# Kernel tuning notes

Measured on AMD Instinct MI355X. Metric: run time of the kernel, lower is better.

The kernel has to match this reference:

```python
import jax, jax.numpy as jnp
import numpy as np

N_MIN = 5
N_MAX = 16
VARIANTS_PER_N = 16
NUM_HIDDEN = 2
HIDDEN = 512
TOTAL_MODELS = (N_MAX - N_MIN + 1) * VARIANTS_PER_N  # 192
BATCH = 65536


def setup_inputs() -> dict:
    key = jax.random.key(0)
    ks = jax.random.split(key, 8)
    n = 16
    s_in = 1.0 / np.sqrt(n)
    s_h = 1.0 / np.sqrt(HIDDEN)
    return {
        "T": jax.random.normal(ks[0], (BATCH, n), dtype=jnp.float32),
        "n": n,
        "variant_index": 3,
        "w_in": jax.random.normal(ks[1], (TOTAL_MODELS, HIDDEN, N_MAX), dtype=jnp.float32) * s_in,
        "b_in": jax.random.normal(ks[2], (TOTAL_MODELS, HIDDEN), dtype=jnp.float32) * 0.01,
        "w_hid": jax.random.normal(ks[3], (TOTAL_MODELS, NUM_HIDDEN, HIDDEN, HIDDEN), dtype=jnp.float32) * s_h,
        "b_hid": jax.random.normal(ks[4], (TOTAL_MODELS, NUM_HIDDEN, HIDDEN), dtype=jnp.float32) * 0.01,
        "w_out": jax.random.normal(ks[5], (TOTAL_MODELS, N_MAX + 1, HIDDEN), dtype=jnp.float32) * s_h,
        "b_out": jax.random.normal(ks[6], (TOTAL_MODELS, N_MAX + 1), dtype=jnp.float32) * 0.01,
    }


def _distortion(X, n):
    # X: (B, n+1). Z[:, n-1-i] = sum_j X[:, j] * X[:, j+i+1] (zero-padded shift).
    # lag k = i+1 -> column n-k; loop is over fixed small n (<=16), unrolls statically.
    cols = [jnp.sum(X[:, :-k] * X[:, k:], axis=1) for k in range(1, n + 1)]
    return jnp.stack(cols[::-1], axis=1)  # (B, n)


def reference(T, n, variant_index, w_in, b_in, w_hid, b_hid, w_out, b_out):
    model_idx = (n - N_MIN) * VARIANTS_PER_N + variant_index
    wi = w_in[model_idx]    # (H, N_MAX)
    bi = b_in[model_idx]    # (H,)
    wh = w_hid[model_idx]   # (2, H, H)
    bh = b_hid[model_idx]   # (2, H)
    wo = w_out[model_idx]   # (N_MAX+1, H)
    bo = b_out[model_idx]   # (N_MAX+1,)

    T_pad = jnp.pad(T, ((0, 0), (0, N_MAX - n)))  # (B, N_MAX)
    norm = jnp.sqrt(jnp.clip(jnp.sum(T_pad * T_pad, axis=1, keepdims=True), 1e-12))
    T_unit = T_pad / norm
    scale = jnp.sqrt(norm)

    x = jax.nn.silu(T_unit @ wi.T + bi)
    for h in range(NUM_HIDDEN):
        x = jax.nn.relu(x @ wh[h].T + bh[h])
    x_full = (x @ wo.T + bo) * scale  # (B, N_MAX+1)

    X_hat = x_full[:, :n + 1]
    X_hat_clamped = jnp.clip(X_hat, -2.0, 2.0)
    error = jnp.mean((_distortion(X_hat, n) - T) ** 2)
    error_clamped = jnp.mean((_distortion(X_hat_clamped, n) - T) ** 2)
    return (X_hat, error, X_hat_clamped, error_clamped)
```

## Files before the change

kernel.cpp:

```cpp
#include <hip/hip_runtime.h>

#define BATCH 65536
#define MT 64

typedef unsigned short u16;
typedef __bf16 bf16x8 __attribute__((ext_vector_type(8)));
typedef float f32x4 __attribute__((ext_vector_type(4)));

#define WI_OFF 0
#define WH_OFF 16384
#define WO_OFF 540672
#define WS_USH 557056
#define BI_F 0
#define BH_F 512
#define BO_F 1536
#define ERR_F 1568
#define PREP_WH 65536
#define PREP_WI 2048
#define PREP_WO 2048
#define PREP_SC 1570
#define PREP_TOTAL (PREP_WH + PREP_WI + PREP_WO + PREP_SC)

__device__ inline u16 f2bf(float f) {
  union { float f; unsigned u; } v; v.f = f;
  unsigned u = v.u + 0x7fffu + ((v.u >> 16) & 1u);
  return (u16)(u >> 16);
}

__global__ void prep_kernel(const float* __restrict__ w_in, const float* __restrict__ b_in,
                            const float* __restrict__ w_hid, const float* __restrict__ b_hid,
                            const float* __restrict__ w_out, const float* __restrict__ b_out,
                            const int* __restrict__ variant, int n,
                            u16* __restrict__ wsu, float* __restrict__ wsf)
{
  const int model = (n - 5) * 16 + variant[0];
  const int i = blockIdx.x * 256 + threadIdx.x;
  if (i < PREP_WH) {
    int g = i & 3, col = (i >> 2) & 511, K32 = (i >> 11) & 15, l = i >> 15;
    const float* src = w_hid + (size_t)model * 524288 + (size_t)l * 262144 + col * 512 + K32 * 32 + g * 8;
    u16* dst = wsu + WH_OFF + (size_t)i * 8;
    #pragma unroll
    for (int e = 0; e < 8; ++e) dst[e] = f2bf(src[e]);
  } else if (i < PREP_WH + PREP_WI) {
    int j = i - PREP_WH;
    int g = j & 3, col = j >> 2;
    u16* dst = wsu + WI_OFF + (size_t)j * 8;
    #pragma unroll
    for (int e = 0; e < 8; ++e) {
      int k = g * 8 + e;
      dst[e] = (k < 16) ? f2bf(w_in[(size_t)model * 8192 + col * 16 + k]) : (u16)0;
    }
  } else if (i < PREP_WH + PREP_WI + PREP_WO) {
    int j = i - PREP_WH - PREP_WI;
    int g = j & 3, col = (j >> 2) & 31, K32 = j >> 7;
    u16* dst = wsu + WO_OFF + (size_t)j * 8;
    #pragma unroll
    for (int e = 0; e < 8; ++e) {
      int k = K32 * 32 + g * 8 + e;
      dst[e] = (col < 17) ? f2bf(w_out[(size_t)model * 8704 + col * 512 + k]) : (u16)0;
    }
  } else if (i < PREP_TOTAL) {
    int j = i - PREP_WH - PREP_WI - PREP_WO;
    if (j < 512)       wsf[BI_F + j] = b_in[(size_t)model * 512 + j];
    else if (j < 1536) wsf[BH_F + (j - 512)] = b_hid[(size_t)model * 1024 + (j - 512)];
    else if (j < 1568) { int o = j - 1536; wsf[BO_F + o] = (o < 17) ? b_out[(size_t)model * 17 + o] : 0.f; }
    else               wsf[ERR_F + (j - 1568)] = 0.f;
  }
}

__device__ __forceinline__ bf16x8 rdA(const char* xb, int row, int kbyte) {
  return *reinterpret_cast<const bf16x8*>(xb + row * 1024 + (kbyte ^ ((row & 15) << 4)));
}
__device__ __forceinline__ void st16(char* xb, int row, int col, u16 v) {
  *(u16*)(xb + row * 1024 + ((col * 2) ^ ((row & 15) << 4))) = v;
}

template<int NK>
__device__ __forceinline__ void dense_layer(const u16* __restrict__ Wp,
                                            const float* __restrict__ bias, int act,
                                            char* xb, int l15, int q, int c0)
{
  f32x4 acc[4][4];
  #pragma unroll
  for (int a = 0; a < 4; ++a)
    #pragma unroll
    for (int b = 0; b < 4; ++b) { f32x4 z = {0.f, 0.f, 0.f, 0.f}; acc[a][b] = z; }

  const u16* Wl = Wp + (c0 + l15) * 32 + q * 8;
  uint4 b0[4], b1[4];
  #pragma unroll
  for (int ct = 0; ct < 4; ++ct)
    b0[ct] = *reinterpret_cast<const uint4*>(Wl + ct * 512);

  #pragma unroll
  for (int K2 = 0; K2 < NK; K2 += 2) {
    if (K2 + 1 < NK) {
      #pragma unroll
      for (int ct = 0; ct < 4; ++ct)
        b1[ct] = *reinterpret_cast<const uint4*>(Wl + (K2 + 1) * 16384 + ct * 512);
    }
    {
      const int kbyte = K2 * 64 + q * 16;
      #pragma unroll
      for (int mt = 0; mt < 4; ++mt) {
        bf16x8 a = rdA(xb, mt * 16 + l15, kbyte);
        #pragma unroll
        for (int ct = 0; ct < 4; ++ct)
          acc[mt][ct] = __builtin_amdgcn_mfma_f32_16x16x32_bf16(
              a, __builtin_bit_cast(bf16x8, b0[ct]), acc[mt][ct], 0, 0, 0);
      }
    }
    if (K2 + 1 < NK) {
      if (K2 + 2 < NK) {
        #pragma unroll
        for (int ct = 0; ct < 4; ++ct)
          b0[ct] = *reinterpret_cast<const uint4*>(Wl + (K2 + 2) * 16384 + ct * 512);
      }
      const int kbyte = (K2 + 1) * 64 + q * 16;
      #pragma unroll
      for (int mt = 0; mt < 4; ++mt) {
        bf16x8 a = rdA(xb, mt * 16 + l15, kbyte);
        #pragma unroll
        for (int ct = 0; ct < 4; ++ct)
          acc[mt][ct] = __builtin_amdgcn_mfma_f32_16x16x32_bf16(
              a, __builtin_bit_cast(bf16x8, b1[ct]), acc[mt][ct], 0, 0, 0);
      }
    }
  }
  __syncthreads();

  float bv[4];
  #pragma unroll
  for (int ct = 0; ct < 4; ++ct) bv[ct] = bias[c0 + ct * 16 + l15];
  #pragma unroll
  for (int mt = 0; mt < 4; ++mt)
    #pragma unroll
    for (int ct = 0; ct < 4; ++ct)
      #pragma unroll
      for (int j = 0; j < 4; ++j) {
        int row = mt * 16 + q * 4 + j;
        float z = acc[mt][ct][j] + bv[ct];
        float h = act ? fmaxf(z, 0.f) : z / (1.f + __expf(-z));
        st16(xb, row, c0 + ct * 16 + l15, f2bf(h));
      }
  __syncthreads();
}

template<int CN>
__global__ __launch_bounds__(512, 2) void fused_kernel(
    const float* __restrict__ T, const u16* __restrict__ wsu,
    const float* __restrict__ wsf, float* __restrict__ Xout, float* __restrict__ Xcout,
    float* __restrict__ errAcc, int n_arg)
{
  const int n = CN ? CN : n_arg;
  __shared__ u16 xs[MT * 512];
  __shared__ float xo[MT * 20];
  __shared__ float scaleS[MT];
  __shared__ float ered[8][2];

  const int tid = threadIdx.x;
  const int blk = blockIdx.x;
  const int lane = tid & 63;
  const int wid = tid >> 6;
  const int l15 = lane & 15;
  const int q = lane >> 4;
  const int c0 = wid * 64;
  char* xb = (char*)xs;

  {
    const int r = tid >> 3, j = tid & 7;
    const size_t gr = (size_t)blk * MT + r;
    const float* tp = T + gr * n;
    const int k0 = 2 * j, k1 = 2 * j + 1;
    float v0 = (k0 < n) ? tp[k0] : 0.f;
    float v1 = (k1 < n) ? tp[k1] : 0.f;
    float ss = v0 * v0 + v1 * v1;
    ss += __shfl_xor(ss, 1); ss += __shfl_xor(ss, 2); ss += __shfl_xor(ss, 4);
    float norm = sqrtf(ss < 1e-12f ? 1e-12f : ss);
    float rn = 1.f / norm;
    if (j == 0) scaleS[r] = sqrtf(norm);
    st16(xb, r, k0, f2bf(v0 * rn));
    st16(xb, r, k1, f2bf(v1 * rn));
    st16(xb, r, 16 + k0, 0);
    st16(xb, r, 16 + k1, 0);
  }
  __syncthreads();

  dense_layer<1 >(wsu + WI_OFF,          wsf + BI_F,       0, xb, l15, q, c0);
  dense_layer<16>(wsu + WH_OFF,          wsf + BH_F,       1, xb, l15, q, c0);
  dense_layer<16>(wsu + WH_OFF + 262144, wsf + BH_F + 512, 1, xb, l15, q, c0);

  if (wid < 4) {
    f32x4 oacc[2];
    { f32x4 z = {0.f, 0.f, 0.f, 0.f}; oacc[0] = z; oacc[1] = z; }
    const int bofs2 = l15 * 32 + q * 8;
    uint4 ob[2], on[2];
    #pragma unroll
    for (int ct = 0; ct < 2; ++ct)
      ob[ct] = *reinterpret_cast<const uint4*>(wsu + WO_OFF + bofs2 + ct * 512);
    #pragma unroll
    for (int K2 = 0; K2 < 16; K2 += 2) {
      #pragma unroll
      for (int ct = 0; ct < 2; ++ct)
        on[ct] = *reinterpret_cast<const uint4*>(wsu + WO_OFF + (K2 + 1) * 1024 + bofs2 + ct * 512);
      {
        bf16x8 a = rdA(xb, wid * 16 + l15, K2 * 64 + q * 16);
        #pragma unroll
        for (int ct = 0; ct < 2; ++ct)
          oacc[ct] = __builtin_amdgcn_mfma_f32_16x16x32_bf16(
              a, __builtin_bit_cast(bf16x8, ob[ct]), oacc[ct], 0, 0, 0);
      }
      if (K2 + 2 < 16) {
        #pragma unroll
        for (int ct = 0; ct < 2; ++ct)
          ob[ct] = *reinterpret_cast<const uint4*>(wsu + WO_OFF + (K2 + 2) * 1024 + bofs2 + ct * 512);
      }
      {
        bf16x8 a = rdA(xb, wid * 16 + l15, (K2 + 1) * 64 + q * 16);
        #pragma unroll
        for (int ct = 0; ct < 2; ++ct)
          oacc[ct] = __builtin_amdgcn_mfma_f32_16x16x32_bf16(
              a, __builtin_bit_cast(bf16x8, on[ct]), oacc[ct], 0, 0, 0);
      }
    }
    #pragma unroll
    for (int ct = 0; ct < 2; ++ct)
      #pragma unroll
      for (int j = 0; j < 4; ++j) {
        int o = ct * 16 + l15;
        int row = wid * 16 + q * 4 + j;
        if (o <= n) {
          float val = (oacc[ct][j] + wsf[BO_F + o]) * scaleS[row];
          size_t gr = (size_t)blk * MT + row;
          float cv = fminf(fmaxf(val, -2.f), 2.f);
          Xout[gr * (n + 1) + o] = val;
          Xcout[gr * (n + 1) + o] = cv;
          xo[row * 20 + o] = val;
        }
      }
  }
  __syncthreads();

  {
    const int r = tid >> 3, j = tid & 7;
    const size_t gr = (size_t)blk * MT + r;
    float x[17], cx[17];
    #pragma unroll
    for (int i = 0; i < 17; ++i) {
      float v = (i <= n) ? xo[r * 20 + i] : 0.f;
      x[i] = v; cx[i] = fminf(fmaxf(v, -2.f), 2.f);
    }
    float e = 0.f, ec = 0.f;
    #pragma unroll
    for (int kk = 0; kk < 2; ++kk) {
      int k = j + 1 + kk * 8;
      if (k <= n) {
        float d = 0.f, dc = 0.f;
        #pragma unroll
        for (int i = 0; i < 16; ++i) {
          if (i + k <= 16) {
            if (i + k <= n) { d += x[i] * x[i + k]; dc += cx[i] * cx[i + k]; }
          }
        }
        float tvv = T[gr * n + (n - k)];
        float r1 = d - tvv, r2 = dc - tvv;
        e += r1 * r1; ec += r2 * r2;
      }
    }
    e += __shfl_xor(e, 1);  ec += __shfl_xor(ec, 1);
    e += __shfl_xor(e, 2);  ec += __shfl_xor(ec, 2);
    e += __shfl_xor(e, 4);  ec += __shfl_xor(ec, 4);
    e += __shfl_xor(e, 8);  ec += __shfl_xor(ec, 8);
    e += __shfl_xor(e, 16); ec += __shfl_xor(ec, 16);
    e += __shfl_xor(e, 32); ec += __shfl_xor(ec, 32);
    if (lane == 0) { ered[wid][0] = e; ered[wid][1] = ec; }
  }
  __syncthreads();
  if (tid == 0) {
    float e = 0.f, ec = 0.f;
    #pragma unroll
    for (int w = 0; w < 8; ++w) { e += ered[w][0]; ec += ered[w][1]; }
    atomicAdd(&errAcc[0], e);
    atomicAdd(&errAcc[1], ec);
  }
}

__global__ void finalize_kernel(const float* __restrict__ errAcc, float* __restrict__ e0,
                                float* __restrict__ e1, float inv)
{
  e0[0] = errAcc[0] * inv;
  e1[0] = errAcc[1] * inv;
}

extern "C" void kernel_launch(void* const* d_in, const int* in_sizes, int n_in,
                              void* d_out, int out_size, void* d_ws, size_t ws_size,
                              hipStream_t stream)
{
  const float* T       = (const float*)d_in[0];
  const int*   variant = (const int*)d_in[2];
  const float* w_in    = (const float*)d_in[3];
  const float* b_in    = (const float*)d_in[4];
  const float* w_hid   = (const float*)d_in[5];
  const float* b_hid   = (const float*)d_in[6];
  const float* w_out   = (const float*)d_in[7];
  const float* b_out   = (const float*)d_in[8];
  const int n = in_sizes[0] / BATCH;

  u16* wsu = (u16*)d_ws;
  float* wsf = (float*)((char*)d_ws + (size_t)WS_USH * 2);
  float* out = (float*)d_out;
  const size_t xe = (size_t)BATCH * (n + 1);
  float* Xo  = out;
  float* eP  = out + xe;
  float* Xc  = out + xe + 1;
  float* ecP = out + 2 * xe + 1;

  const int prepBlocks = (PREP_TOTAL + 255) / 256;
  prep_kernel<<<prepBlocks, 256, 0, stream>>>(w_in, b_in, w_hid, b_hid, w_out, b_out,
                                              variant, n, wsu, wsf);
  if (n == 16)
    fused_kernel<16><<<BATCH / MT, 512, 0, stream>>>(T, wsu, wsf, Xo, Xc, wsf + ERR_F, n);
  else
    fused_kernel<0><<<BATCH / MT, 512, 0, stream>>>(T, wsu, wsf, Xo, Xc, wsf + ERR_F, n);
  finalize_kernel<<<1, 1, 0, stream>>>(wsf + ERR_F, eP, ecP, 1.f / (float)((size_t)BATCH * n));
}
```

Baseline: 139.0 us.

## Double row tile to 128 with 1024-thread blocks and stagger K order per block

The row tile grows from 64 to 128. Blocks now run 1024 threads as 16 waves arranged as two row halves by eight column slices, so each weight fragment loaded into registers is shared across twice as many rows per block. The K iteration order in the hidden layers is rotated by a per-block offset, spreading concurrent blocks over different parts of the weight matrix in cache. The costs are double the LDS per block, which limits occupancy to about one block per CU. The aggressive launch bounds may also force register limits or spills.

```diff
diff --git a/kernel.cpp b/kernel.cpp
--- a/kernel.cpp
+++ b/kernel.cpp
@@ -1,7 +1,7 @@
 #include <hip/hip_runtime.h>
 
 #define BATCH 65536
-#define MT 64
+#define MT 128
 
 typedef unsigned short u16;
 typedef __bf16 bf16x8 __attribute__((ext_vector_type(8)));
@@ -78,7 +78,7 @@
 template<int NK>
 __device__ __forceinline__ void dense_layer(const u16* __restrict__ Wp,
                                             const float* __restrict__ bias, int act,
-                                            char* xb, int l15, int q, int c0)
+                                            char* xb, int l15, int q, int r0, int c0, int koff)
 {
   f32x4 acc[4][4];
   #pragma unroll
@@ -88,38 +88,43 @@
 
   const u16* Wl = Wp + (c0 + l15) * 32 + q * 8;
   uint4 b0[4], b1[4];
+  {
+    const u16* p = Wl + (size_t)((koff) & (NK - 1)) * 16384;
+    #pragma unroll
+    for (int ct = 0; ct < 4; ++ct)
+      b0[ct] = *reinterpret_cast<const uint4*>(p + ct * 512);
+  }
+
   #pragma unroll
-  for (int ct = 0; ct < 4; ++ct)
-    b0[ct] = *reinterpret_cast<const uint4*>(Wl + ct * 512);
-
-  #pragma unroll
-  for (int K2 = 0; K2 < NK; K2 += 2) {
-    if (K2 + 1 < NK) {
+  for (int i = 0; i < NK; i += 2) {
+    if (i + 1 < NK) {
+      const u16* p = Wl + (size_t)((i + 1 + koff) & (NK - 1)) * 16384;
       #pragma unroll
       for (int ct = 0; ct < 4; ++ct)
-        b1[ct] = *reinterpret_cast<const uint4*>(Wl + (K2 + 1) * 16384 + ct * 512);
+        b1[ct] = *reinterpret_cast<const uint4*>(p + ct * 512);
     }
     {
-      const int kbyte = K2 * 64 + q * 16;
+      const int kb = ((i + koff) & (NK - 1)) * 64 + q * 16;
       #pragma unroll
       for (int mt = 0; mt < 4; ++mt) {
-        bf16x8 a = rdA(xb, mt * 16 + l15, kbyte);
+        bf16x8 a = rdA(xb, r0 + mt * 16 + l15, kb);
         #pragma unroll
         for (int ct = 0; ct < 4; ++ct)
           acc[mt][ct] = __builtin_amdgcn_mfma_f32_16x16x32_bf16(
               a, __builtin_bit_cast(bf16x8, b0[ct]), acc[mt][ct], 0, 0, 0);
       }
     }
-    if (K2 + 1 < NK) {
-      if (K2 + 2 < NK) {
+    if (i + 1 < NK) {
+      if (i + 2 < NK) {
+        const u16* p = Wl + (size_t)((i + 2 + koff) & (NK - 1)) * 16384;
         #pragma unroll
         for (int ct = 0; ct < 4; ++ct)
-          b0[ct] = *reinterpret_cast<const uint4*>(Wl + (K2 + 2) * 16384 + ct * 512);
-      }
-      const int kbyte = (K2 + 1) * 64 + q * 16;
+          b0[ct] = *reinterpret_cast<const uint4*>(p + ct * 512);
+      }
+      const int kb = ((i + 1 + koff) & (NK - 1)) * 64 + q * 16;
       #pragma unroll
       for (int mt = 0; mt < 4; ++mt) {
-        bf16x8 a = rdA(xb, mt * 16 + l15, kbyte);
+        bf16x8 a = rdA(xb, r0 + mt * 16 + l15, kb);
         #pragma unroll
         for (int ct = 0; ct < 4; ++ct)
           acc[mt][ct] = __builtin_amdgcn_mfma_f32_16x16x32_bf16(
@@ -138,7 +143,7 @@
     for (int ct = 0; ct < 4; ++ct)
       #pragma unroll
       for (int j = 0; j < 4; ++j) {
-        int row = mt * 16 + q * 4 + j;
+        int row = r0 + mt * 16 + q * 4 + j;
         float z = acc[mt][ct][j] + bv[ct];
         float h = act ? fmaxf(z, 0.f) : z / (1.f + __expf(-z));
         st16(xb, row, c0 + ct * 16 + l15, f2bf(h));
@@ -147,7 +152,7 @@
 }
 
 template<int CN>
-__global__ __launch_bounds__(512, 2) void fused_kernel(
+__global__ __launch_bounds__(1024, 4) void fused_kernel(
     const float* __restrict__ T, const u16* __restrict__ wsu,
     const float* __restrict__ wsf, float* __restrict__ Xout, float* __restrict__ Xcout,
     float* __restrict__ errAcc, int n_arg)
@@ -156,7 +161,7 @@
   __shared__ u16 xs[MT * 512];
   __shared__ float xo[MT * 20];
   __shared__ float scaleS[MT];
-  __shared__ float ered[8][2];
+  __shared__ float ered[16][2];
 
   const int tid = threadIdx.x;
   const int blk = blockIdx.x;
@@ -164,7 +169,9 @@
   const int wid = tid >> 6;
   const int l15 = lane & 15;
   const int q = lane >> 4;
-  const int c0 = wid * 64;
+  const int r0 = (wid >> 3) * 64;
+  const int c0 = (wid & 7) * 64;
+  const int koff = (blk >> 3) & 15;
   char* xb = (char*)xs;
 
   {
@@ -186,11 +193,11 @@
   }
   __syncthreads();
 
-  dense_layer<1 >(wsu + WI_OFF,          wsf + BI_F,       0, xb, l15, q, c0);
-  dense_layer<16>(wsu + WH_OFF,          wsf + BH_F,       1, xb, l15, q, c0);
-  dense_layer<16>(wsu + WH_OFF + 262144, wsf + BH_F + 512, 1, xb, l15, q, c0);
-
-  if (wid < 4) {
+  dense_layer<1 >(wsu + WI_OFF,          wsf + BI_F,       0, xb, l15, q, r0, c0, 0);
+  dense_layer<16>(wsu + WH_OFF,          wsf + BH_F,       1, xb, l15, q, r0, c0, koff);
+  dense_layer<16>(wsu + WH_OFF + 262144, wsf + BH_F + 512, 1, xb, l15, q, r0, c0, koff);
+
+  if (wid < 8) {
     f32x4 oacc[2];
     { f32x4 z = {0.f, 0.f, 0.f, 0.f}; oacc[0] = z; oacc[1] = z; }
     const int bofs2 = l15 * 32 + q * 8;
@@ -279,7 +286,7 @@
   if (tid == 0) {
     float e = 0.f, ec = 0.f;
     #pragma unroll
-    for (int w = 0; w < 8; ++w) { e += ered[w][0]; ec += ered[w][1]; }
+    for (int w = 0; w < 16; ++w) { e += ered[w][0]; ec += ered[w][1]; }
     atomicAdd(&errAcc[0], e);
     atomicAdd(&errAcc[1], ec);
   }
@@ -319,8 +326,8 @@
   prep_kernel<<<prepBlocks, 256, 0, stream>>>(w_in, b_in, w_hid, b_hid, w_out, b_out,
                                               variant, n, wsu, wsf);
   if (n == 16)
-    fused_kernel<16><<<BATCH / MT, 512, 0, stream>>>(T, wsu, wsf, Xo, Xc, wsf + ERR_F, n);
+    fused_kernel<16><<<BATCH / MT, 1024, 0, stream>>>(T, wsu, wsf, Xo, Xc, wsf + ERR_F, n);
   else
-    fused_kernel<0><<<BATCH / MT, 512, 0, stream>>>(T, wsu, wsf, Xo, Xc, wsf + ERR_F, n);
+    fused_kernel<0><<<BATCH / MT, 1024, 0, stream>>>(T, wsu, wsf, Xo, Xc, wsf + ERR_F, n);
   finalize_kernel<<<1, 1, 0, stream>>>(wsf + ERR_F, eP, ecP, 1.f / (float)((size_t)BATCH * n));
 }
```

After: 190.7 us. 37.2% more time.

## Stagger K order per block, raise occupancy bound, replace atomics with partial reduction

Applied to the files above, without the earlier changes.

The hidden-layer GEMM loop now starts at a block-dependent K offset and wraps around, so concurrent blocks read different weight slices instead of all hitting the same addresses. The loop is no longer unrolled, and the launch bound rises to 4 blocks per CU to allow more occupancy. Per-block error partials are written to workspace and reduced in a 256-thread finalize kernel instead of global atomics. The risks are register pressure under the tighter bound (possible spills) and loop overhead from the non-unrolled loop.

```diff
diff --git a/kernel.cpp b/kernel.cpp
--- a/kernel.cpp
+++ b/kernel.cpp
@@ -14,11 +14,11 @@
 #define BI_F 0
 #define BH_F 512
 #define BO_F 1536
-#define ERR_F 1568
+#define PART_F 1568
 #define PREP_WH 65536
 #define PREP_WI 2048
 #define PREP_WO 2048
-#define PREP_SC 1570
+#define PREP_SC 1568
 #define PREP_TOTAL (PREP_WH + PREP_WI + PREP_WO + PREP_SC)
 
 __device__ inline u16 f2bf(float f) {
@@ -63,8 +63,7 @@
     int j = i - PREP_WH - PREP_WI - PREP_WO;
     if (j < 512)       wsf[BI_F + j] = b_in[(size_t)model * 512 + j];
     else if (j < 1536) wsf[BH_F + (j - 512)] = b_hid[(size_t)model * 1024 + (j - 512)];
-    else if (j < 1568) { int o = j - 1536; wsf[BO_F + o] = (o < 17) ? b_out[(size_t)model * 17 + o] : 0.f; }
-    else               wsf[ERR_F + (j - 1568)] = 0.f;
+    else               { int o = j - 1536; wsf[BO_F + o] = (o < 17) ? b_out[(size_t)model * 17 + o] : 0.f; }
   }
 }
 
@@ -78,7 +77,7 @@
 template<int NK>
 __device__ __forceinline__ void dense_layer(const u16* __restrict__ Wp,
                                             const float* __restrict__ bias, int act,
-                                            char* xb, int l15, int q, int c0)
+                                            char* xb, int l15, int q, int c0, int koff)
 {
   f32x4 acc[4][4];
   #pragma unroll
@@ -87,43 +86,66 @@
     for (int b = 0; b < 4; ++b) { f32x4 z = {0.f, 0.f, 0.f, 0.f}; acc[a][b] = z; }
 
   const u16* Wl = Wp + (c0 + l15) * 32 + q * 8;
-  uint4 b0[4], b1[4];
-  #pragma unroll
-  for (int ct = 0; ct < 4; ++ct)
-    b0[ct] = *reinterpret_cast<const uint4*>(Wl + ct * 512);
-
-  #pragma unroll
-  for (int K2 = 0; K2 < NK; K2 += 2) {
-    if (K2 + 1 < NK) {
+
+  if constexpr (NK == 1) {
+    uint4 b0[4];
+    #pragma unroll
+    for (int ct = 0; ct < 4; ++ct)
+      b0[ct] = *reinterpret_cast<const uint4*>(Wl + ct * 512);
+    const int kb = q * 16;
+    #pragma unroll
+    for (int mt = 0; mt < 4; ++mt) {
+      bf16x8 a = rdA(xb, mt * 16 + l15, kb);
       #pragma unroll
       for (int ct = 0; ct < 4; ++ct)
-        b1[ct] = *reinterpret_cast<const uint4*>(Wl + (K2 + 1) * 16384 + ct * 512);
-    }
+        acc[mt][ct] = __builtin_amdgcn_mfma_f32_16x16x32_bf16(
+            a, __builtin_bit_cast(bf16x8, b0[ct]), acc[mt][ct], 0, 0, 0);
+    }
+  } else {
+    uint4 bc[4], bn[4];
     {
-      const int kbyte = K2 * 64 + q * 16;
-      #pragma unroll
-      for (int mt = 0; mt < 4; ++mt) {
-        bf16x8 a = rdA(xb, mt * 16 + l15, kbyte);
+      const u16* p = Wl + (size_t)koff * 16384;
+      #pragma unroll
+      for (int ct = 0; ct < 4; ++ct)
+        bc[ct] = *reinterpret_cast<const uint4*>(p + ct * 512);
+    }
+    #pragma unroll 1
+    for (int i = 0; i < NK; i += 2) {
+      {
+        const int Kb = (i + 1) ^ koff;
+        const u16* p = Wl + (size_t)Kb * 16384;
         #pragma unroll
         for (int ct = 0; ct < 4; ++ct)
-          acc[mt][ct] = __builtin_amdgcn_mfma_f32_16x16x32_bf16(
-              a, __builtin_bit_cast(bf16x8, b0[ct]), acc[mt][ct], 0, 0, 0);
-      }
-    }
-    if (K2 + 1 < NK) {
-      if (K2 + 2 < NK) {
+          bn[ct] = *reinterpret_cast<const uint4*>(p + ct * 512);
+      }
+      {
+        const int kb = ((i ^ koff) * 64) + q * 16;
+        #pragma unroll
+        for (int mt = 0; mt < 4; ++mt) {
+          bf16x8 a = rdA(xb, mt * 16 + l15, kb);
+          #pragma unroll
+          for (int ct = 0; ct < 4; ++ct)
+            acc[mt][ct] = __builtin_amdgcn_mfma_f32_16x16x32_bf16(
+                a, __builtin_bit_cast(bf16x8, bc[ct]), acc[mt][ct], 0, 0, 0);
+        }
+      }
+      {
+        const int Kc = ((i + 2) & (NK - 1)) ^ koff;
+        const u16* p = Wl + (size_t)Kc * 16384;
         #pragma unroll
         for (int ct = 0; ct < 4; ++ct)
-          b0[ct] = *reinterpret_cast<const uint4*>(Wl + (K2 + 2) * 16384 + ct * 512);
-      }
-      const int kbyte = (K2 + 1) * 64 + q * 16;
-      #pragma unroll
-      for (int mt = 0; mt < 4; ++mt) {
-        bf16x8 a = rdA(xb, mt * 16 + l15, kbyte);
-        #pragma unroll
-        for (int ct = 0; ct < 4; ++ct)
-          acc[mt][ct] = __builtin_amdgcn_mfma_f32_16x16x32_bf16(
-              a, __builtin_bit_cast(bf16x8, b1[ct]), acc[mt][ct], 0, 0, 0);
+          bc[ct] = *reinterpret_cast<const uint4*>(p + ct * 512);
+      }
+      {
+        const int kb = (((i + 1) ^ koff) * 64) + q * 16;
+        #pragma unroll
+        for (int mt = 0; mt < 4; ++mt) {
+          bf16x8 a = rdA(xb, mt * 16 + l15, kb);
+          #pragma unroll
+          for (int ct = 0; ct < 4; ++ct)
+            acc[mt][ct] = __builtin_amdgcn_mfma_f32_16x16x32_bf16(
+                a, __builtin_bit_cast(bf16x8, bn[ct]), acc[mt][ct], 0, 0, 0);
+        }
       }
     }
   }
@@ -147,10 +169,10 @@
 }
 
 template<int CN>
-__global__ __launch_bounds__(512, 2) void fused_kernel(
+__global__ __launch_bounds__(512, 4) void fused_kernel(
     const float* __restrict__ T, const u16* __restrict__ wsu,
     const float* __restrict__ wsf, float* __restrict__ Xout, float* __restrict__ Xcout,
-    float* __restrict__ errAcc, int n_arg)
+    float* __restrict__ errPart, int n_arg)
 {
   const int n = CN ? CN : n_arg;
   __shared__ u16 xs[MT * 512];
@@ -165,6 +187,7 @@
   const int l15 = lane & 15;
   const int q = lane >> 4;
   const int c0 = wid * 64;
+  const int koff = (blk >> 3) & 15;
   char* xb = (char*)xs;
 
   {
@@ -186,9 +209,9 @@
   }
   __syncthreads();
 
-  dense_layer<1 >(wsu + WI_OFF,          wsf + BI_F,       0, xb, l15, q, c0);
-  dense_layer<16>(wsu + WH_OFF,          wsf + BH_F,       1, xb, l15, q, c0);
-  dense_layer<16>(wsu + WH_OFF + 262144, wsf + BH_F + 512, 1, xb, l15, q, c0);
+  dense_layer<1 >(wsu + WI_OFF,          wsf + BI_F,       0, xb, l15, q, c0, 0);
+  dense_layer<16>(wsu + WH_OFF,          wsf + BH_F,       1, xb, l15, q, c0, koff);
+  dense_layer<16>(wsu + WH_OFF + 262144, wsf + BH_F + 512, 1, xb, l15, q, c0, koff);
 
   if (wid < 4) {
     f32x4 oacc[2];
@@ -280,16 +303,33 @@
     float e = 0.f, ec = 0.f;
     #pragma unroll
     for (int w = 0; w < 8; ++w) { e += ered[w][0]; ec += ered[w][1]; }
-    atomicAdd(&errAcc[0], e);
-    atomicAdd(&errAcc[1], ec);
-  }
-}
-
-__global__ void finalize_kernel(const float* __restrict__ errAcc, float* __restrict__ e0,
+    errPart[blk * 2]     = e;
+    errPart[blk * 2 + 1] = ec;
+  }
+}
+
+__global__ void finalize_kernel(const float* __restrict__ part, float* __restrict__ e0,
                                 float* __restrict__ e1, float inv)
 {
-  e0[0] = errAcc[0] * inv;
-  e1[0] = errAcc[1] * inv;
+  __shared__ float se[4][2];
+  const int t = threadIdx.x;
+  float e = 0.f, ec = 0.f;
+  for (int b = t; b < BATCH / MT; b += 256) { e += part[2 * b]; ec += part[2 * b + 1]; }
+  e += __shfl_xor(e, 1);  ec += __shfl_xor(ec, 1);
+  e += __shfl_xor(e, 2);  ec += __shfl_xor(ec, 2);
+  e += __shfl_xor(e, 4);  ec += __shfl_xor(ec, 4);
+  e += __shfl_xor(e, 8);  ec += __shfl_xor(ec, 8);
+  e += __shfl_xor(e, 16); ec += __shfl_xor(ec, 16);
+  e += __shfl_xor(e, 32); ec += __shfl_xor(ec, 32);
+  if ((t & 63) == 0) { se[t >> 6][0] = e; se[t >> 6][1] = ec; }
+  __syncthreads();
+  if (t == 0) {
+    float te = 0.f, tec = 0.f;
+    #pragma unroll
+    for (int w = 0; w < 4; ++w) { te += se[w][0]; tec += se[w][1]; }
+    e0[0] = te * inv;
+    e1[0] = tec * inv;
+  }
 }
 
 extern "C" void kernel_launch(void* const* d_in, const int* in_sizes, int n_in,
@@ -319,8 +359,8 @@
   prep_kernel<<<prepBlocks, 256, 0, stream>>>(w_in, b_in, w_hid, b_hid, w_out, b_out,
                                               variant, n, wsu, wsf);
   if (n == 16)
-    fused_kernel<16><<<BATCH / MT, 512, 0, stream>>>(T, wsu, wsf, Xo, Xc, wsf + ERR_F, n);
+    fused_kernel<16><<<BATCH / MT, 512, 0, stream>>>(T, wsu, wsf, Xo, Xc, wsf + PART_F, n);
   else
-    fused_kernel<0><<<BATCH / MT, 512, 0, stream>>>(T, wsu, wsf, Xo, Xc, wsf + ERR_F, n);
-  finalize_kernel<<<1, 1, 0, stream>>>(wsf + ERR_F, eP, ecP, 1.f / (float)((size_t)BATCH * n));
-}
+    fused_kernel<0><<<BATCH / MT, 512, 0, stream>>>(T, wsu, wsf, Xo, Xc, wsf + PART_F, n);
+  finalize_kernel<<<1, 256, 0, stream>>>(wsf + PART_F, eP, ecP, 1.f / (float)((size_t)BATCH * n));
+}
```

Result: slower. 145.6 us (+4.7%).
